# Kernel optimization log

Hardware: AMD Instinct MI355X
Metric: run time of the kernel (lower is better)

## Reference

```python
import jax, jax.numpy as jnp
import numpy as np

B, S, H = 64, 4096, 256
NEG = 1e30


def setup_inputs() -> dict:
    key = jax.random.key(0)
    k1, k2, k3, k4, k5 = jax.random.split(key, 5)
    inp_seq = jax.random.normal(k1, (B, S, H), dtype=jnp.float32)
    mask = jax.random.randint(k2, (B, S), 0, 2).astype(jnp.float32)
    mask = mask.at[:, 0].set(1.0)  # ensure at least one valid position per row
    query = jax.random.normal(k3, (B, H), dtype=jnp.float32)
    # nn.Linear(2H, H): weight [H, 2H], bias [H]
    lim = 1.0 / np.sqrt(2 * H)
    W = jax.random.uniform(k4, (H, 2 * H), minval=-lim, maxval=lim, dtype=jnp.float32)
    b = jax.random.uniform(k5, (H,), minval=-lim, maxval=lim, dtype=jnp.float32)
    return {"inp_seq": inp_seq, "mask": mask, "query": query, "W": W, "b": b}


def reference(inp_seq, mask, query, W, b):
    # single-query attention pooling
    score = jnp.einsum("bsh,bh->bs", inp_seq, query)          # [B,S]
    score = score - NEG * (1.0 - mask)                          # additive mask
    att = jax.nn.softmax(score, axis=-1)                        # [B,S]
    extracted_msg = jnp.einsum("bs,bsh->bh", att, inp_seq)     # [B,H]
    conc = jnp.concatenate([query, extracted_msg], axis=1)      # [B,2H]
    control_emb = conc @ W.T + b                                # [B,H]
    return (extracted_msg, control_emb)
```

## Files before the change

kernel.cpp:

```cpp
#include <hip/hip_runtime.h>
#include <math.h>

namespace {
constexpr int kB = 64;
constexpr int kS = 4096;
constexpr int kH = 256;
constexpr int kChunks = 32;
constexpr int kChunkS = kS / kChunks;
constexpr int kWavesPerBlock = 4;
constexpr int kPosPerWave = kChunkS / kWavesPerBlock;
constexpr int kPartStride = kH + 2;
constexpr float kNeg = 1e30f;
}

__global__ __launch_bounds__(256, 8) void pass1_kernel(
    const float* __restrict__ x, const float* __restrict__ mask,
    const float* __restrict__ q, float* __restrict__ part) {
  const int blk = blockIdx.x;
  const int b = blk >> 5;
  const int c = blk & (kChunks - 1);
  const int tid = threadIdx.x;
  const int wave = tid >> 6;
  const int lane = tid & 63;

  const float4 q4 = *reinterpret_cast<const float4*>(q + b * kH + lane * 4);
  const float* xb = x + (size_t)b * kS * kH;
  const float* mrow = mask + b * kS;
  const int s_base = c * kChunkS + wave * kPosPerWave;

  float m = -INFINITY;
  float l = 0.f;
  float4 acc = make_float4(0.f, 0.f, 0.f, 0.f);

  #pragma unroll 4
  for (int i = 0; i < kPosPerWave; ++i) {
    const int s = s_base + i;
    const float4 x4 =
        *reinterpret_cast<const float4*>(xb + (size_t)s * kH + lane * 4);
    float p = x4.x * q4.x + x4.y * q4.y + x4.z * q4.z + x4.w * q4.w;
    #pragma unroll
    for (int off = 32; off > 0; off >>= 1) p += __shfl_xor(p, off, 64);
    const float score = p - kNeg * (1.0f - mrow[s]);
    const float m_new = fmaxf(m, score);
    const float alpha = __expf(m - m_new);
    const float w = __expf(score - m_new);
    l = l * alpha + w;
    acc.x = acc.x * alpha + w * x4.x;
    acc.y = acc.y * alpha + w * x4.y;
    acc.z = acc.z * alpha + w * x4.z;
    acc.w = acc.w * alpha + w * x4.w;
    m = m_new;
  }

  __shared__ float sm[kWavesPerBlock];
  __shared__ float sl[kWavesPerBlock];
  __shared__ float sacc[kWavesPerBlock][kH];
  if (lane == 0) { sm[wave] = m; sl[wave] = l; }
  *reinterpret_cast<float4*>(&sacc[wave][lane * 4]) = acc;
  __syncthreads();

  const float m_b = fmaxf(fmaxf(sm[0], sm[1]), fmaxf(sm[2], sm[3]));
  const float a0 = __expf(sm[0] - m_b);
  const float a1 = __expf(sm[1] - m_b);
  const float a2 = __expf(sm[2] - m_b);
  const float a3 = __expf(sm[3] - m_b);
  float* out = part + (size_t)blk * kPartStride;
  out[tid] = sacc[0][tid] * a0 + sacc[1][tid] * a1 +
             sacc[2][tid] * a2 + sacc[3][tid] * a3;
  if (tid == 0) {
    out[kH] = m_b;
    out[kH + 1] = sl[0] * a0 + sl[1] * a1 + sl[2] * a2 + sl[3] * a3;
  }
}

__global__ __launch_bounds__(256, 4) void pass2_kernel(
    const float* __restrict__ part, const float* __restrict__ q,
    const float* __restrict__ W, const float* __restrict__ bias,
    float* __restrict__ out) {
  const int b = blockIdx.x;
  const int tid = threadIdx.x;

  const float* pb = part + (size_t)b * kChunks * kPartStride;
  float m_g = -INFINITY;
  #pragma unroll
  for (int c = 0; c < kChunks; ++c)
    m_g = fmaxf(m_g, pb[c * kPartStride + kH]);
  float l_g = 0.f, num = 0.f;
  #pragma unroll 4
  for (int c = 0; c < kChunks; ++c) {
    const float* p = pb + c * kPartStride;
    const float scale = __expf(p[kH] - m_g);
    l_g += scale * p[kH + 1];
    num += scale * p[tid];
  }
  const float msg = num / l_g;
  out[(size_t)b * kH + tid] = msg;

  __shared__ float conc[2 * kH];
  conc[tid] = q[b * kH + tid];
  conc[kH + tid] = msg;
  __syncthreads();

  float acc = bias[tid];
  const float* wr = W + (size_t)tid * (2 * kH);
  #pragma unroll 8
  for (int j = 0; j < 2 * kH; j += 4) {
    const float4 w4 = *reinterpret_cast<const float4*>(wr + j);
    acc += conc[j] * w4.x + conc[j + 1] * w4.y +
           conc[j + 2] * w4.z + conc[j + 3] * w4.w;
  }
  out[(size_t)(kB * kH) + (size_t)b * kH + tid] = acc;
}

extern "C" void kernel_launch(void* const* d_in, const int* in_sizes, int n_in,
                              void* d_out, int out_size, void* d_ws, size_t ws_size,
                              hipStream_t stream) {
  const float* x    = (const float*)d_in[0];
  const float* mask = (const float*)d_in[1];
  const float* q    = (const float*)d_in[2];
  const float* W    = (const float*)d_in[3];
  const float* bias = (const float*)d_in[4];
  float* out = (float*)d_out;
  float* part = (float*)d_ws;

  pass1_kernel<<<kB * kChunks, 256, 0, stream>>>(x, mask, q, part);
  pass2_kernel<<<kB, 256, 0, stream>>>(part, q, W, bias, out);
}
```

Baseline: 376.5 us.

## Batch eight positions per online-softmax step with DPP reductions and exp2

The pass-1 loop now loads eight rows of x and eight mask values up front, then computes their scores. It updates the running max and accumulator once per batch of eight instead of once per position. Each wave-wide dot-product reduction uses DPP row shifts and broadcasts plus a readlane, replacing the chain of xor shuffles. Scores are pre-scaled by log2(e) so that hardware exp2 replaces expf, and launch bounds drop to 4 blocks per CU to leave room for the extra registers. The aim is more loads in flight and a shorter serial dependency chain, at the cost of higher register use and lower occupancy.

Result: slower. 438.7 us (+16.5%).

```diff
diff --git a/kernel.cpp b/kernel.cpp
--- a/kernel.cpp
+++ b/kernel.cpp
@@ -9,11 +9,29 @@
 constexpr int kChunkS = kS / kChunks;
 constexpr int kWavesPerBlock = 4;
 constexpr int kPosPerWave = kChunkS / kWavesPerBlock;
+constexpr int kBatch = 8;
+constexpr int kNumBatch = kPosPerWave / kBatch;
 constexpr int kPartStride = kH + 2;
-constexpr float kNeg = 1e30f;
+constexpr float kLog2e = 1.4426950408889634f;
+constexpr float kNegL2 = 1.4426950408889634e30f;
 }
 
-__global__ __launch_bounds__(256, 8) void pass1_kernel(
+__device__ __forceinline__ float dpp_sum64(float x) {
+  float f = x;
+#define DPP_STEP(ctrl)                                                     \
+  f += __int_as_float(__builtin_amdgcn_update_dpp(                         \
+      0, __float_as_int(f), ctrl, 0xF, 0xF, true))
+  DPP_STEP(0x111);
+  DPP_STEP(0x112);
+  DPP_STEP(0x114);
+  DPP_STEP(0x118);
+  DPP_STEP(0x142);
+  DPP_STEP(0x143);
+#undef DPP_STEP
+  return __int_as_float(__builtin_amdgcn_readlane(__float_as_int(f), 63));
+}
+
+__global__ __launch_bounds__(256, 4) void pass1_kernel(
     const float* __restrict__ x, const float* __restrict__ mask,
     const float* __restrict__ q, float* __restrict__ part) {
   const int blk = blockIdx.x;
@@ -24,31 +42,59 @@
   const int lane = tid & 63;
 
   const float4 q4 = *reinterpret_cast<const float4*>(q + b * kH + lane * 4);
-  const float* xb = x + (size_t)b * kS * kH;
-  const float* mrow = mask + b * kS;
   const int s_base = c * kChunkS + wave * kPosPerWave;
+  const float* xw = x + ((size_t)b * kS + s_base) * kH + lane * 4;
+  const float* mrow = mask + b * kS + s_base;
 
   float m = -INFINITY;
   float l = 0.f;
   float4 acc = make_float4(0.f, 0.f, 0.f, 0.f);
 
-  #pragma unroll 4
-  for (int i = 0; i < kPosPerWave; ++i) {
-    const int s = s_base + i;
-    const float4 x4 =
-        *reinterpret_cast<const float4*>(xb + (size_t)s * kH + lane * 4);
-    float p = x4.x * q4.x + x4.y * q4.y + x4.z * q4.z + x4.w * q4.w;
+  #pragma unroll
+  for (int i = 0; i < kNumBatch; ++i) {
+    float4 xb[kBatch];
     #pragma unroll
-    for (int off = 32; off > 0; off >>= 1) p += __shfl_xor(p, off, 64);
-    const float score = p - kNeg * (1.0f - mrow[s]);
-    const float m_new = fmaxf(m, score);
-    const float alpha = __expf(m - m_new);
-    const float w = __expf(score - m_new);
-    l = l * alpha + w;
-    acc.x = acc.x * alpha + w * x4.x;
-    acc.y = acc.y * alpha + w * x4.y;
-    acc.z = acc.z * alpha + w * x4.z;
-    acc.w = acc.w * alpha + w * x4.w;
+    for (int j = 0; j < kBatch; ++j)
+      xb[j] = *reinterpret_cast<const float4*>(xw + (i * kBatch + j) * kH);
+    const float4 mk0 = *reinterpret_cast<const float4*>(mrow + i * kBatch);
+    const float4 mk1 = *reinterpret_cast<const float4*>(mrow + i * kBatch + 4);
+    const float bias[kBatch] = {
+        (mk0.x - 1.f) * kNegL2, (mk0.y - 1.f) * kNegL2,
+        (mk0.z - 1.f) * kNegL2, (mk0.w - 1.f) * kNegL2,
+        (mk1.x - 1.f) * kNegL2, (mk1.y - 1.f) * kNegL2,
+        (mk1.z - 1.f) * kNegL2, (mk1.w - 1.f) * kNegL2};
+
+    float s2[kBatch];
+    #pragma unroll
+    for (int j = 0; j < kBatch; ++j) {
+      const float p = xb[j].x * q4.x + xb[j].y * q4.y +
+                      xb[j].z * q4.z + xb[j].w * q4.w;
+      s2[j] = fmaf(dpp_sum64(p), kLog2e, bias[j]);
+    }
+
+    float M = s2[0];
+    #pragma unroll
+    for (int j = 1; j < kBatch; ++j) M = fmaxf(M, s2[j]);
+    const float m_new = fmaxf(m, M);
+    const float alpha = __builtin_amdgcn_exp2f(m - m_new);
+    float w[kBatch];
+    float wsum = 0.f;
+    #pragma unroll
+    for (int j = 0; j < kBatch; ++j) {
+      w[j] = __builtin_amdgcn_exp2f(s2[j] - m_new);
+      wsum += w[j];
+    }
+    l = fmaf(l, alpha, wsum);
+    float ax = acc.x * alpha, ay = acc.y * alpha;
+    float az = acc.z * alpha, aw = acc.w * alpha;
+    #pragma unroll
+    for (int j = 0; j < kBatch; ++j) {
+      ax = fmaf(w[j], xb[j].x, ax);
+      ay = fmaf(w[j], xb[j].y, ay);
+      az = fmaf(w[j], xb[j].z, az);
+      aw = fmaf(w[j], xb[j].w, aw);
+    }
+    acc = make_float4(ax, ay, az, aw);
     m = m_new;
   }
 
@@ -60,10 +106,10 @@
   __syncthreads();
 
   const float m_b = fmaxf(fmaxf(sm[0], sm[1]), fmaxf(sm[2], sm[3]));
-  const float a0 = __expf(sm[0] - m_b);
-  const float a1 = __expf(sm[1] - m_b);
-  const float a2 = __expf(sm[2] - m_b);
-  const float a3 = __expf(sm[3] - m_b);
+  const float a0 = __builtin_amdgcn_exp2f(sm[0] - m_b);
+  const float a1 = __builtin_amdgcn_exp2f(sm[1] - m_b);
+  const float a2 = __builtin_amdgcn_exp2f(sm[2] - m_b);
+  const float a3 = __builtin_amdgcn_exp2f(sm[3] - m_b);
   float* out = part + (size_t)blk * kPartStride;
   out[tid] = sacc[0][tid] * a0 + sacc[1][tid] * a1 +
              sacc[2][tid] * a2 + sacc[3][tid] * a3;
@@ -89,7 +135,7 @@
   #pragma unroll 4
   for (int c = 0; c < kChunks; ++c) {
     const float* p = pb + c * kPartStride;
-    const float scale = __expf(p[kH] - m_g);
+    const float scale = __builtin_amdgcn_exp2f(p[kH] - m_g);
     l_g += scale * p[kH + 1];
     num += scale * p[tid];
   }
```
